# Optimization experiments

Hardware: AMD Instinct MI355X
Metric: run time of the kernel (lower is better)

## Reference

```python
import jax, jax.numpy as jnp
import numpy as np

NUM_NODES = 100000
EMBED_DIM = 64
NUM_EDGES = 1200000
NUM_LAYERS = 3
ALPHA = 0.25  # 1 / (num_layers + 1)


def setup_inputs() -> dict:
    key = jax.random.key(0)
    k1, k2, k3, k4 = jax.random.split(key, 4)
    x = jax.random.normal(k1, (NUM_NODES, EMBED_DIM), dtype=jnp.float32)
    edge_attr = jax.random.uniform(k2, (NUM_EDGES,), dtype=jnp.float32)
    edge_index = jax.random.randint(k3, (2, NUM_EDGES), 0, NUM_NODES, dtype=jnp.int64)
    edge_mask = jax.random.randint(k4, (NUM_EDGES,), 0, 2, dtype=jnp.int32).astype(jnp.bool_)
    return {"x": x, "edge_attr": edge_attr, "edge_index": edge_index, "edge_mask": edge_mask}


def reference(x, edge_attr, edge_index, edge_mask):
    # Masked edge selection == zeroing masked edge weights (same degree & aggregation).
    w = edge_attr * edge_mask.astype(edge_attr.dtype)  # [E]
    row, col = edge_index[0], edge_index[1]            # source, target

    # gcn_norm with add_self_loops=False: D^{-1/2} A D^{-1/2}
    deg = jax.ops.segment_sum(w, col, num_segments=NUM_NODES)          # [N]
    dinv = jnp.where(deg > 0, jax.lax.rsqrt(deg), 0.0)                 # [N]
    norm = dinv[row] * w * dinv[col]                                   # [E]

    out = ALPHA * x
    h = x
    for _ in range(NUM_LAYERS):
        msg = norm[:, None] * h[row]                                   # [E, D] gather
        h = jax.ops.segment_sum(msg, col, num_segments=NUM_NODES)      # [N, D] scatter
        out = out + ALPHA * h
    return out
```

## Files before the change

### kernel.cpp

```cpp
#include <hip/hip_runtime.h>
#include <hip/hip_fp16.h>

#define N_NODES 100000
#define EMB     64
#define N_EDGES 1200000
#define N_EPAD  (N_EDGES + 3 * N_NODES + 64)
#define ALPHA   0.25f
#define SCAN_CHUNK 1024
#define NPART ((N_NODES + SCAN_CHUNK - 1) / SCAN_CHUNK)

__global__ void k_detect(const unsigned char* __restrict__ maskB,
                         const int* __restrict__ idx, int* __restrict__ flags) {
    int tid = blockIdx.x * blockDim.x + threadIdx.x;
    int lane = threadIdx.x & 63;
    bool mev = (tid & 3) && maskB[tid];
    if (__any(mev) && lane == 0) atomicOr(&flags[0], 1);
    bool iev = (tid < 4096) && (idx[2 * tid + 1] != 0);
    if (__any(iev) && lane == 0) atomicOr(&flags[1], 1);
}

__device__ __forceinline__ int idx_row(const int* idx, int i64, int e) {
    return i64 ? idx[2 * e] : idx[e];
}
__device__ __forceinline__ int idx_col(const int* idx, int i64, int e) {
    return i64 ? idx[2 * (N_EDGES + e)] : idx[N_EDGES + e];
}
__device__ __forceinline__ int edge_mask(const void* maskp, int mbool, int e) {
    return mbool ? (int)((const unsigned char*)maskp)[e] : ((const int*)maskp)[e];
}

__global__ void k_hist(const float* __restrict__ ea, const void* maskp,
                       const int* __restrict__ idx, const int* __restrict__ flags,
                       int* __restrict__ cnt, int* __restrict__ rank) {
    int e = blockIdx.x * blockDim.x + threadIdx.x;
    if (e >= N_EDGES) return;
    int mbool = flags[0] != 0, i64 = (flags[1] == 0);
    if (!edge_mask(maskp, mbool, e)) return;
    float wv = ea[e];
    if (wv == 0.0f) return;
    int c = idx_col(idx, i64, e);
    if ((unsigned)c >= N_NODES) return;
    rank[e] = atomicAdd(&cnt[c], 1);
}

__global__ void k_scanx(const int* __restrict__ cnt, int* __restrict__ gTotal,
                        int* __restrict__ row_start, int2* __restrict__ csr) {
    __shared__ int sh[256];
    __shared__ int sbase;
    int tid = threadIdx.x;
    int base = blockIdx.x * SCAN_CHUNK + tid * 4;
    int v[4], p[4];
    int s = 0;
#pragma unroll
    for (int k = 0; k < 4; ++k) {
        int i = base + k;
        v[k] = (i < N_NODES) ? cnt[i] : 0;
        if (v[k] < 0) v[k] = 0;
        p[k] = (v[k] + 3) & ~3;
        s += p[k];
    }
    sh[tid] = s;
    __syncthreads();
    for (int d = 1; d < 256; d <<= 1) {
        int t = (tid >= d) ? sh[tid - d] : 0;
        __syncthreads();
        sh[tid] += t;
        __syncthreads();
    }
    if (tid == 255) sbase = atomicAdd(gTotal, sh[255]);
    __syncthreads();
    int off = sbase + sh[tid] - s;
#pragma unroll
    for (int k = 0; k < 4; ++k) {
        int i = base + k;
        if (i < N_NODES) {
            row_start[i] = off;
            for (int z = v[k]; z < p[k]; ++z)
                if ((unsigned)(off + z) < N_EPAD) csr[off + z] = make_int2(0, 0);
            off += p[k];
        }
    }
}

__global__ void k_fill(const float* __restrict__ ea, const void* maskp,
                       const int* __restrict__ idx, const int* __restrict__ flags,
                       const int* __restrict__ row_start, const int* __restrict__ rank,
                       int2* __restrict__ csr) {
    int e = blockIdx.x * blockDim.x + threadIdx.x;
    if (e >= N_EDGES) return;
    int mbool = flags[0] != 0, i64 = (flags[1] == 0);
    if (!edge_mask(maskp, mbool, e)) return;
    float wv = ea[e];
    if (wv == 0.0f) return;
    int c = idx_col(idx, i64, e);
    if ((unsigned)c >= N_NODES) return;
    int r = idx_row(idx, i64, e);
    int rok = (unsigned)r < N_NODES;
    int p = row_start[c] + rank[e];
    if ((unsigned)p < N_EPAD)
        csr[p] = make_int2(__float_as_int(rok ? wv : 0.0f), rok ? r : 0);
}

__global__ __launch_bounds__(256) void k_degconv(
        const int* __restrict__ row_start, const int* __restrict__ cnt,
        const int2* __restrict__ csr, const float4* __restrict__ x4,
        float4* __restrict__ t0, float* __restrict__ dinv, float* __restrict__ sd) {
    int t = blockIdx.x * blockDim.x + threadIdx.x;
    int n = t >> 3;
    int q = t & 7;
    if (n >= N_NODES) return;
    int beg = row_start[n];
    int c = cnt[n];
    if (c < 0) c = 0;
    int pc = (c + 3) & ~3;
    float s = 0.0f;
    for (int j = q; j < pc; j += 8) s += __int_as_float(csr[beg + j].x);
    s += __shfl_xor(s, 1);
    s += __shfl_xor(s, 2);
    s += __shfl_xor(s, 4);
    float di = (s > 0.0f) ? rsqrtf(s) : 0.0f;
    if (q == 0) {
        dinv[n] = di;
        sd[n] = (s > 0.0f) ? sqrtf(s) : 0.0f;
    }
    size_t xb = (size_t)n * 16 + q * 2;
    float4 v0 = x4[xb], v1 = x4[xb + 1];
    float4 o;
    __half2* op = reinterpret_cast<__half2*>(&o);
    op[0] = __floats2half2_rn(di * v0.x, di * v0.y);
    op[1] = __floats2half2_rn(di * v0.z, di * v0.w);
    op[2] = __floats2half2_rn(di * v1.x, di * v1.y);
    op[3] = __floats2half2_rn(di * v1.z, di * v1.w);
    t0[(size_t)n * 8 + q] = o;
}

__device__ __forceinline__ void accum_h8(float4& sa, float4& sb, float w,
                                         float4 raw) {
    const __half2* hp = reinterpret_cast<const __half2*>(&raw);
    float2 f0 = __half22float2(hp[0]);
    float2 f1 = __half22float2(hp[1]);
    float2 f2 = __half22float2(hp[2]);
    float2 f3 = __half22float2(hp[3]);
    sa.x += w * f0.x; sa.y += w * f0.y; sa.z += w * f1.x; sa.w += w * f1.y;
    sb.x += w * f2.x; sb.y += w * f2.y; sb.z += w * f3.x; sb.w += w * f3.y;
}

__device__ __forceinline__ void gather_core_f16(
        const int* __restrict__ row_start, const int* __restrict__ cnt,
        const int2* __restrict__ csr, const float4* __restrict__ h16,
        int n, int q, float4& sa, float4& sb) {
    sa = make_float4(0.f, 0.f, 0.f, 0.f);
    sb = make_float4(0.f, 0.f, 0.f, 0.f);
    int beg = row_start[n];
    int c = cnt[n];
    if (c <= 0) return;
    int nb = ((c + 3) & ~3) >> 2;
    const int4* csr4 = (const int4*)(csr + beg);
    for (int t = 0; t < nb; ++t) {
        int4 pa = csr4[2 * t];
        int4 pb = csr4[2 * t + 1];
        float w0 = __int_as_float(pa.x);
        float w1 = __int_as_float(pa.z);
        float w2 = __int_as_float(pb.x);
        float w3 = __int_as_float(pb.z);
        int r0 = min((unsigned)pa.y, (unsigned)(N_NODES - 1));
        int r1 = min((unsigned)pa.w, (unsigned)(N_NODES - 1));
        int r2 = min((unsigned)pb.y, (unsigned)(N_NODES - 1));
        int r3 = min((unsigned)pb.w, (unsigned)(N_NODES - 1));
        float4 v0 = h16[(size_t)r0 * 8 + q];
        float4 v1 = h16[(size_t)r1 * 8 + q];
        float4 v2 = h16[(size_t)r2 * 8 + q];
        float4 v3 = h16[(size_t)r3 * 8 + q];
        accum_h8(sa, sb, w0, v0);
        accum_h8(sa, sb, w1, v1);
        accum_h8(sa, sb, w2, v2);
        accum_h8(sa, sb, w3, v3);
    }
}

__global__ __launch_bounds__(256, 6) void k_gather_mid(
        const int* __restrict__ row_start, const int* __restrict__ cnt,
        const int2* __restrict__ csr, const float* __restrict__ dinv,
        const float4* __restrict__ tsrc, float4* __restrict__ tdst) {
    int t = blockIdx.x * blockDim.x + threadIdx.x;
    int n = t >> 3;
    int q = t & 7;
    if (n >= N_NODES) return;
    float4 sa, sb;
    gather_core_f16(row_start, cnt, csr, tsrc, n, q, sa, sb);
    float di = dinv[n];
    float d2 = di * di;
    float4 o;
    __half2* op = reinterpret_cast<__half2*>(&o);
    op[0] = __floats2half2_rn(d2 * sa.x, d2 * sa.y);
    op[1] = __floats2half2_rn(d2 * sa.z, d2 * sa.w);
    op[2] = __floats2half2_rn(d2 * sb.x, d2 * sb.y);
    op[3] = __floats2half2_rn(d2 * sb.z, d2 * sb.w);
    tdst[(size_t)n * 8 + q] = o;
}

__global__ __launch_bounds__(256, 6) void k_gather_last(
        const int* __restrict__ row_start, const int* __restrict__ cnt,
        const int2* __restrict__ csr, const float* __restrict__ dinv,
        const float* __restrict__ sd,
        const float4* __restrict__ x4, const float4* __restrict__ t1_16,
        const float4* __restrict__ t2_16, float4* __restrict__ out4) {
    int t = blockIdx.x * blockDim.x + threadIdx.x;
    int n = t >> 3;
    int q = t & 7;
    if (n >= N_NODES) return;
    float4 sa, sb;
    gather_core_f16(row_start, cnt, csr, t2_16, n, q, sa, sb);
    float di = dinv[n];
    float sdv = sd[n];
    size_t o8 = (size_t)n * 8 + q;
    float4 r1 = t1_16[o8];
    float4 r2 = t2_16[o8];
    const __half2* a1 = reinterpret_cast<const __half2*>(&r1);
    const __half2* a2 = reinterpret_cast<const __half2*>(&r2);
    float2 b10 = __half22float2(a1[0]), b11 = __half22float2(a1[1]);
    float2 b12 = __half22float2(a1[2]), b13 = __half22float2(a1[3]);
    float2 b20 = __half22float2(a2[0]), b21 = __half22float2(a2[1]);
    float2 b22 = __half22float2(a2[2]), b23 = __half22float2(a2[3]);
    size_t ox = (size_t)n * 16 + 2 * q;
    float4 x0 = x4[ox], x1 = x4[ox + 1];
    float4 o0, o1;
    o0.x = ALPHA * (x0.x + sdv * (b10.x + b20.x) + di * sa.x);
    o0.y = ALPHA * (x0.y + sdv * (b10.y + b20.y) + di * sa.y);
    o0.z = ALPHA * (x0.z + sdv * (b11.x + b21.x) + di * sa.z);
    o0.w = ALPHA * (x0.w + sdv * (b11.y + b21.y) + di * sa.w);
    o1.x = ALPHA * (x1.x + sdv * (b12.x + b22.x) + di * sb.x);
    o1.y = ALPHA * (x1.y + sdv * (b12.y + b22.y) + di * sb.y);
    o1.z = ALPHA * (x1.z + sdv * (b13.x + b23.x) + di * sb.z);
    o1.w = ALPHA * (x1.w + sdv * (b13.y + b23.y) + di * sb.w);
    out4[ox] = o0;
    out4[ox + 1] = o1;
}

extern "C" void kernel_launch(void* const* d_in, const int* in_sizes, int n_in,
                              void* d_out, int out_size, void* d_ws, size_t ws_size,
                              hipStream_t stream) {
    const float* x   = (const float*)d_in[0];
    const float* ea  = (const float*)d_in[1];
    const int*   idx = (const int*)d_in[2];
    const void*  msk = d_in[3];
    float*       out = (float*)d_out;

    char* ws = (char*)d_ws;
    size_t off = 0;
    auto alloc = [&](size_t bytes) -> void* {
        void* p = ws + off;
        off = (off + bytes + 255) & ~(size_t)255;
        return p;
    };
    int*    flags     = (int*)   alloc(64);
    int*    cnt       = (int*)   alloc(sizeof(int)   * N_NODES);
    int*    row_start = (int*)   alloc(sizeof(int)   * N_NODES);
    float*  dinv      = (float*) alloc(sizeof(float) * N_NODES);
    float*  sd        = (float*) alloc(sizeof(float) * N_NODES);
    int*    rank      = (int*)   alloc(sizeof(int)   * N_EDGES);
    int2*   csr       = (int2*)  alloc(sizeof(int2)  * N_EPAD);
    float4* t0        = (float4*)alloc(sizeof(unsigned short) * (size_t)N_NODES * EMB);
    float4* tA        = (float4*)alloc(sizeof(unsigned short) * (size_t)N_NODES * EMB);
    float4* tB        = (float4*)alloc(sizeof(unsigned short) * (size_t)N_NODES * EMB);
    int*    gTotal    = flags + 8;

    const int B = 256;
    const int gE = (N_EDGES + B - 1) / B;
    const int gG = (N_NODES * 8 + B - 1) / B;

    (void)hipMemsetAsync(flags, 0, (size_t)((char*)row_start - (char*)flags), stream);
    k_detect <<<64, 256, 0, stream>>>((const unsigned char*)msk, idx, flags);
    k_hist   <<<gE, B, 0, stream>>>(ea, msk, idx, flags, cnt, rank);
    k_scanx  <<<NPART, 256, 0, stream>>>(cnt, gTotal, row_start, csr);
    k_fill   <<<gE, B, 0, stream>>>(ea, msk, idx, flags, row_start, rank, csr);
    k_degconv<<<gG, B, 0, stream>>>(row_start, cnt, csr, (const float4*)x,
                                    t0, dinv, sd);

    k_gather_mid <<<gG, B, 0, stream>>>(row_start, cnt, csr, dinv, t0, tA);
    k_gather_mid <<<gG, B, 0, stream>>>(row_start, cnt, csr, dinv, tA, tB);
    k_gather_last<<<gG, B, 0, stream>>>(row_start, cnt, csr, dinv, sd,
                                        (const float4*)x, tA, tB, (float4*)out);
}
```

Measured before the change: 194.7 us.

## Build fixed-capacity per-node edge slots in one pass with overflow CSR fallback

Replaces the histogram, scan and fill passes with one kernel that atomically ranks each edge and writes it straight into a fixed 32-slot-per-node staging array. The scan and fill kernels become a fallback that runs only when some node's degree exceeds the cap. This removes one full pass over the edges, the rank buffer and the scan from the common path. The cost is a larger, sparser slot array (100000×32 int2) whose scattered rows may hurt gather locality, plus dropping the occupancy hint on the gather kernels.

```diff
diff --git a/kernel.cpp b/kernel.cpp
--- a/kernel.cpp
+++ b/kernel.cpp
@@ -4,6 +4,7 @@
 #define N_NODES 100000
 #define EMB     64
 #define N_EDGES 1200000
+#define CAP     32
 #define N_EPAD  (N_EDGES + 3 * N_NODES + 64)
 #define ALPHA   0.25f
 #define SCAN_CHUNK 1024
@@ -29,9 +30,9 @@
     return mbool ? (int)((const unsigned char*)maskp)[e] : ((const int*)maskp)[e];
 }
 
-__global__ void k_hist(const float* __restrict__ ea, const void* maskp,
-                       const int* __restrict__ idx, const int* __restrict__ flags,
-                       int* __restrict__ cnt, int* __restrict__ rank) {
+__global__ void k_histfill(const float* __restrict__ ea, const void* maskp,
+                           const int* __restrict__ idx, int* flags,
+                           int* __restrict__ cnt, int2* __restrict__ staged) {
     int e = blockIdx.x * blockDim.x + threadIdx.x;
     if (e >= N_EDGES) return;
     int mbool = flags[0] != 0, i64 = (flags[1] == 0);
@@ -40,11 +41,20 @@
     if (wv == 0.0f) return;
     int c = idx_col(idx, i64, e);
     if ((unsigned)c >= N_NODES) return;
-    rank[e] = atomicAdd(&cnt[c], 1);
-}
-
-__global__ void k_scanx(const int* __restrict__ cnt, int* __restrict__ gTotal,
-                        int* __restrict__ row_start, int2* __restrict__ csr) {
+    int r = idx_row(idx, i64, e);
+    int rok = (unsigned)r < N_NODES;
+    int rank = atomicAdd(&cnt[c], 1);
+    if (rank < CAP)
+        staged[c * CAP + rank] = make_int2(__float_as_int(rok ? wv : 0.0f),
+                                           rok ? r : 0);
+    else
+        atomicOr(&flags[2], 1);
+}
+
+__global__ void k_scan_ovf(const int* flags, const int* __restrict__ cnt,
+                           int* __restrict__ gTotal, int* __restrict__ row_start,
+                           int2* __restrict__ csr2) {
+    if (flags[2] == 0) return;
     __shared__ int sh[256];
     __shared__ int sbase;
     int tid = threadIdx.x;
@@ -76,16 +86,17 @@
         if (i < N_NODES) {
             row_start[i] = off;
             for (int z = v[k]; z < p[k]; ++z)
-                if ((unsigned)(off + z) < N_EPAD) csr[off + z] = make_int2(0, 0);
+                if ((unsigned)(off + z) < N_EPAD) csr2[off + z] = make_int2(0, 0);
             off += p[k];
         }
     }
 }
 
-__global__ void k_fill(const float* __restrict__ ea, const void* maskp,
-                       const int* __restrict__ idx, const int* __restrict__ flags,
-                       const int* __restrict__ row_start, const int* __restrict__ rank,
-                       int2* __restrict__ csr) {
+__global__ void k_fill_ovf(const float* __restrict__ ea, const void* maskp,
+                           const int* __restrict__ idx, const int* flags,
+                           const int* __restrict__ row_start,
+                           int* __restrict__ cnt2, int2* __restrict__ csr2) {
+    if (flags[2] == 0) return;
     int e = blockIdx.x * blockDim.x + threadIdx.x;
     if (e >= N_EDGES) return;
     int mbool = flags[0] != 0, i64 = (flags[1] == 0);
@@ -96,28 +107,38 @@
     if ((unsigned)c >= N_NODES) return;
     int r = idx_row(idx, i64, e);
     int rok = (unsigned)r < N_NODES;
-    int p = row_start[c] + rank[e];
+    int p = row_start[c] + atomicAdd(&cnt2[c], 1);
     if ((unsigned)p < N_EPAD)
-        csr[p] = make_int2(__float_as_int(rok ? wv : 0.0f), rok ? r : 0);
+        csr2[p] = make_int2(__float_as_int(rok ? wv : 0.0f), rok ? r : 0);
+}
+
+__device__ __forceinline__ const int2* slice_base(
+        int ovf, const int* __restrict__ row_start,
+        const int2* __restrict__ staged, const int2* __restrict__ csr2, int n) {
+    return ovf ? (csr2 + row_start[n]) : (staged + n * CAP);
 }
 
 __global__ __launch_bounds__(256) void k_degconv(
-        const int* __restrict__ row_start, const int* __restrict__ cnt,
-        const int2* __restrict__ csr, const float4* __restrict__ x4,
+        const int* flags, const int* __restrict__ row_start,
+        const int* __restrict__ cnt, int2* __restrict__ staged,
+        int2* __restrict__ csr2, const float4* __restrict__ x4,
         float4* __restrict__ t0, float* __restrict__ dinv, float* __restrict__ sd) {
     int t = blockIdx.x * blockDim.x + threadIdx.x;
     int n = t >> 3;
     int q = t & 7;
     if (n >= N_NODES) return;
-    int beg = row_start[n];
+    int ovf = flags[2];
     int c = cnt[n];
     if (c < 0) c = 0;
-    int pc = (c + 3) & ~3;
+    if (!ovf && c > CAP) c = CAP;
+    int2* base = (int2*)slice_base(ovf, row_start, staged, csr2, n);
     float s = 0.0f;
-    for (int j = q; j < pc; j += 8) s += __int_as_float(csr[beg + j].x);
+    for (int j = q; j < c; j += 8) s += __int_as_float(base[j].x);
     s += __shfl_xor(s, 1);
     s += __shfl_xor(s, 2);
     s += __shfl_xor(s, 4);
+    int pc = (c + 3) & ~3;
+    if (q < pc - c) base[c + q] = make_int2(0, 0);
     float di = (s > 0.0f) ? rsqrtf(s) : 0.0f;
     if (q == 0) {
         dinv[n] = di;
@@ -146,16 +167,13 @@
 }
 
 __device__ __forceinline__ void gather_core_f16(
-        const int* __restrict__ row_start, const int* __restrict__ cnt,
-        const int2* __restrict__ csr, const float4* __restrict__ h16,
-        int n, int q, float4& sa, float4& sb) {
+        const int2* __restrict__ base, int c, const float4* __restrict__ h16,
+        int q, float4& sa, float4& sb) {
     sa = make_float4(0.f, 0.f, 0.f, 0.f);
     sb = make_float4(0.f, 0.f, 0.f, 0.f);
-    int beg = row_start[n];
-    int c = cnt[n];
     if (c <= 0) return;
     int nb = ((c + 3) & ~3) >> 2;
-    const int4* csr4 = (const int4*)(csr + beg);
+    const int4* csr4 = (const int4*)base;
     for (int t = 0; t < nb; ++t) {
         int4 pa = csr4[2 * t];
         int4 pb = csr4[2 * t + 1];
@@ -178,16 +196,21 @@
     }
 }
 
-__global__ __launch_bounds__(256, 6) void k_gather_mid(
-        const int* __restrict__ row_start, const int* __restrict__ cnt,
-        const int2* __restrict__ csr, const float* __restrict__ dinv,
+__global__ __launch_bounds__(256) void k_gather_mid(
+        const int* flags, const int* __restrict__ row_start,
+        const int* __restrict__ cnt, const int2* __restrict__ staged,
+        const int2* __restrict__ csr2, const float* __restrict__ dinv,
         const float4* __restrict__ tsrc, float4* __restrict__ tdst) {
     int t = blockIdx.x * blockDim.x + threadIdx.x;
     int n = t >> 3;
     int q = t & 7;
     if (n >= N_NODES) return;
+    int ovf = flags[2];
+    int c = cnt[n];
+    if (!ovf && c > CAP) c = CAP;
+    const int2* base = slice_base(ovf, row_start, staged, csr2, n);
     float4 sa, sb;
-    gather_core_f16(row_start, cnt, csr, tsrc, n, q, sa, sb);
+    gather_core_f16(base, c, tsrc, q, sa, sb);
     float di = dinv[n];
     float d2 = di * di;
     float4 o;
@@ -199,9 +222,10 @@
     tdst[(size_t)n * 8 + q] = o;
 }
 
-__global__ __launch_bounds__(256, 6) void k_gather_last(
-        const int* __restrict__ row_start, const int* __restrict__ cnt,
-        const int2* __restrict__ csr, const float* __restrict__ dinv,
+__global__ __launch_bounds__(256) void k_gather_last(
+        const int* flags, const int* __restrict__ row_start,
+        const int* __restrict__ cnt, const int2* __restrict__ staged,
+        const int2* __restrict__ csr2, const float* __restrict__ dinv,
         const float* __restrict__ sd,
         const float4* __restrict__ x4, const float4* __restrict__ t1_16,
         const float4* __restrict__ t2_16, float4* __restrict__ out4) {
@@ -209,8 +233,12 @@
     int n = t >> 3;
     int q = t & 7;
     if (n >= N_NODES) return;
+    int ovf = flags[2];
+    int c = cnt[n];
+    if (!ovf && c > CAP) c = CAP;
+    const int2* base = slice_base(ovf, row_start, staged, csr2, n);
     float4 sa, sb;
-    gather_core_f16(row_start, cnt, csr, t2_16, n, q, sa, sb);
+    gather_core_f16(base, c, t2_16, q, sa, sb);
     float di = dinv[n];
     float sdv = sd[n];
     size_t o8 = (size_t)n * 8 + q;
@@ -255,11 +283,12 @@
     };
     int*    flags     = (int*)   alloc(64);
     int*    cnt       = (int*)   alloc(sizeof(int)   * N_NODES);
+    int*    cnt2      = (int*)   alloc(sizeof(int)   * N_NODES);
     int*    row_start = (int*)   alloc(sizeof(int)   * N_NODES);
     float*  dinv      = (float*) alloc(sizeof(float) * N_NODES);
     float*  sd        = (float*) alloc(sizeof(float) * N_NODES);
-    int*    rank      = (int*)   alloc(sizeof(int)   * N_EDGES);
-    int2*   csr       = (int2*)  alloc(sizeof(int2)  * N_EPAD);
+    int2*   staged    = (int2*)  alloc(sizeof(int2)  * (size_t)N_NODES * CAP);
+    int2*   csr2      = (int2*)  alloc(sizeof(int2)  * N_EPAD);
     float4* t0        = (float4*)alloc(sizeof(unsigned short) * (size_t)N_NODES * EMB);
     float4* tA        = (float4*)alloc(sizeof(unsigned short) * (size_t)N_NODES * EMB);
     float4* tB        = (float4*)alloc(sizeof(unsigned short) * (size_t)N_NODES * EMB);
@@ -270,15 +299,18 @@
     const int gG = (N_NODES * 8 + B - 1) / B;
 
     (void)hipMemsetAsync(flags, 0, (size_t)((char*)row_start - (char*)flags), stream);
-    k_detect <<<64, 256, 0, stream>>>((const unsigned char*)msk, idx, flags);
-    k_hist   <<<gE, B, 0, stream>>>(ea, msk, idx, flags, cnt, rank);
-    k_scanx  <<<NPART, 256, 0, stream>>>(cnt, gTotal, row_start, csr);
-    k_fill   <<<gE, B, 0, stream>>>(ea, msk, idx, flags, row_start, rank, csr);
-    k_degconv<<<gG, B, 0, stream>>>(row_start, cnt, csr, (const float4*)x,
-                                    t0, dinv, sd);
-
-    k_gather_mid <<<gG, B, 0, stream>>>(row_start, cnt, csr, dinv, t0, tA);
-    k_gather_mid <<<gG, B, 0, stream>>>(row_start, cnt, csr, dinv, tA, tB);
-    k_gather_last<<<gG, B, 0, stream>>>(row_start, cnt, csr, dinv, sd,
-                                        (const float4*)x, tA, tB, (float4*)out);
-}
+    k_detect  <<<64, 256, 0, stream>>>((const unsigned char*)msk, idx, flags);
+    k_histfill<<<gE, B, 0, stream>>>(ea, msk, idx, flags, cnt, staged);
+    k_scan_ovf<<<NPART, 256, 0, stream>>>(flags, cnt, gTotal, row_start, csr2);
+    k_fill_ovf<<<gE, B, 0, stream>>>(ea, msk, idx, flags, row_start, cnt2, csr2);
+    k_degconv <<<gG, B, 0, stream>>>(flags, row_start, cnt, staged, csr2,
+                                     (const float4*)x, t0, dinv, sd);
+
+    k_gather_mid <<<gG, B, 0, stream>>>(flags, row_start, cnt, staged, csr2,
+                                        dinv, t0, tA);
+    k_gather_mid <<<gG, B, 0, stream>>>(flags, row_start, cnt, staged, csr2,
+                                        dinv, tA, tB);
+    k_gather_last<<<gG, B, 0, stream>>>(flags, row_start, cnt, staged, csr2,
+                                        dinv, sd, (const float4*)x, tA, tB,
+                                        (float4*)out);
+}
```

Result: no change. 193.3 us (-0.7%).
